# Kernel optimization log

Measured on AMD Instinct MI355X. Metric: run time of the kernel, lower is better.

Reference implementation:

```python
import jax, jax.numpy as jnp
import numpy as np


def setup_inputs() -> dict:
    key = jax.random.key(0)
    k1, k2 = jax.random.split(key)
    b, c, h, w = 8, 256, 96, 192
    x = jax.random.normal(k1, (b, c, h, w), dtype=jnp.float32)
    y = jax.random.normal(k2, (b, c, h, w), dtype=jnp.float32)
    return {"x": x, "y": y, "max_displacement": 4}


def _correlation(x, y, md):
    # x, y: [B, C, H, W]. Output: [B, K*K, H, W], K = 2*md+1.
    b, c, h, w = x.shape
    K = 2 * md + 1
    # zero-pad y spatially so out-of-bounds displacements contribute 0
    yp = jnp.pad(y, ((0, 0), (0, 0), (md, md), (md, md)))
    # fixed small loop over K*K displacements (81 for md=4)
    outs = [
        jnp.einsum('bchw,bchw->bhw', x, yp[:, :, di:di + h, dj:dj + w])
        for di in range(K) for dj in range(K)
    ]
    out = jnp.stack(outs, axis=1)  # [B, K*K, H, W]
    return out / c


def reference(x, y, max_displacement):
    return _correlation(x, y, max_displacement)
```

## Files before the change

kernel.cpp:

```cpp
#include <hip/hip_runtime.h>
#include <hip/hip_bf16.h>
#include <stdint.h>


using f32x4 = __attribute__((ext_vector_type(4))) float;
using s16x4 = __attribute__((ext_vector_type(4))) short;
using u16x4 = __attribute__((ext_vector_type(4))) unsigned short;

#define C_DIM 256
#define H_DIM 96
#define W_DIM 192
#define HWSZ  (H_DIM * W_DIM)
#define MD 4
#define KD 9
#define CHUNK 16
#define NCHUNK (C_DIM / CHUNK)
#define HR 8
#define NTHR 512
#define WTILES 12
#define HQ 12
#define SUB_B 128
#define YROW_B (8 * SUB_B)
#define XROW_B (4 * SUB_B)
#define YSZ    (16 * YROW_B)
#define XBASE  YSZ
#define BUFSZ  (YSZ + 8 * XROW_B)
#define LDS_BYTES (2 * BUFSZ)

static __device__ __forceinline__ unsigned short bf16b(float f) {
  __bf16 h = (__bf16)f;
  unsigned short s; __builtin_memcpy(&s, &h, 2); return s;
}

static __device__ __forceinline__ s16x4 tr16(uint32_t addr) {
  s16x4 d;
  asm volatile("ds_read_b64_tr_b16 %0, %1" : "=v"(d) : "v"(addr));
  return d;
}

__global__ __launch_bounds__(NTHR, 4)
void corr_mfma(const float* __restrict__ xg, const float* __restrict__ yg,
               float* __restrict__ outg) {
  __shared__ __align__(16) char smem[LDS_BYTES];

  const int bid = blockIdx.x;
  const int b   = bid & 7;
  const int rem = bid >> 3;
  const int wt  = rem / HQ;
  const int hq  = rem - wt * HQ;
  const int w0  = wt * 16;
  const int h0  = hq * HR;

  const int tid  = threadIdx.x;
  const int lane = tid & 63;
  const int wv   = tid >> 6;
  const int hi   = lane >> 4;
  const int lm   = lane & 15;

  const uint32_t sbase = (uint32_t)(uintptr_t)&smem[0];

  uint32_t goffY[3], loffY[3], goffX, loffX;
  uint32_t vmY = 0;
#pragma unroll
  for (int i = 0; i < 3; ++i) {
    const int qid = i * NTHR + tid;
    const int q = qid % 6;
    const int c = (qid / 6) & 15;
    const int r = qid / 96;
    const int hg = h0 + r - MD;
    const int sg = w0 - MD + 4 * q;
    const bool ok = (hg >= 0) && (hg < H_DIM) && (sg >= 0) && (sg < W_DIM);
    if (ok) vmY |= (1u << i);
    goffY[i] = ok ? (uint32_t)(((b * C_DIM + c) * H_DIM + hg) * W_DIM + sg) : 0u;
    const int s = 4 * q;
    loffY[i] = r * YROW_B + (s >> 4) * 512 + (c >> 2) * SUB_B + (c & 3) * 32 + (s & 15) * 2;
  }
  {
    const int q = tid & 3;
    const int c = (tid >> 2) & 15;
    const int r = tid >> 6;
    goffX = (uint32_t)(((b * C_DIM + c) * H_DIM + (h0 + r)) * W_DIM + (w0 + 4 * q));
    loffX = XBASE + r * XROW_B + (c >> 2) * SUB_B + (c & 3) * 32 + 8 * q;
  }

  f32x4 acc[KD][2];
#pragma unroll
  for (int di = 0; di < KD; ++di) {
    acc[di][0] = f32x4{0.f, 0.f, 0.f, 0.f};
    acc[di][1] = f32x4{0.f, 0.f, 0.f, 0.f};
  }

  const uint32_t abase = sbase + XBASE + wv * XROW_B + hi * SUB_B + lm * 8;
  const uint32_t bbase = sbase + wv * YROW_B + hi * SUB_B + lm * 8;

  float4 v[4];
  u16x4  wreg[4];

#pragma unroll
  for (int i = 0; i < 3; ++i) {
    float4 t4 = make_float4(0.f, 0.f, 0.f, 0.f);
    if (vmY & (1u << i)) t4 = *(const float4*)(yg + goffY[i]);
    v[i] = t4;
  }
  v[3] = *(const float4*)(xg + goffX);
#pragma unroll
  for (int i = 0; i < 4; ++i)
    wreg[i] = u16x4{bf16b(v[i].x), bf16b(v[i].y), bf16b(v[i].z), bf16b(v[i].w)};
#pragma unroll
  for (int i = 0; i < 3; ++i) *(u16x4*)(smem + loffY[i]) = wreg[i];
  *(u16x4*)(smem + loffX) = wreg[3];
  __syncthreads();

  for (int t = 0; t < NCHUNK; ++t) {
    if (t + 1 < NCHUNK) {
      const uint32_t co = (uint32_t)(t + 1) * CHUNK * HWSZ;
#pragma unroll
      for (int i = 0; i < 3; ++i) {
        float4 t4 = make_float4(0.f, 0.f, 0.f, 0.f);
        if (vmY & (1u << i)) t4 = *(const float4*)(yg + goffY[i] + co);
        v[i] = t4;
      }
      v[3] = *(const float4*)(xg + goffX + co);
    }

    const uint32_t bo = (uint32_t)(t & 1) * BUFSZ;
    s16x4 afr = tr16(abase + bo);
    s16x4 b0 = tr16(bbase + bo);
    s16x4 b1 = tr16(bbase + bo + 512);
#pragma unroll
    for (int di = 0; di < KD; ++di) {
      s16x4 n0, n1;
      if (di < 8) {
        const uint32_t bb = bbase + bo + (uint32_t)(di + 1) * YROW_B;
        n0 = tr16(bb);
        n1 = tr16(bb + 512);
        asm volatile("s_waitcnt lgkmcnt(2)" ::: "memory");
      } else {
        asm volatile("s_waitcnt lgkmcnt(0)" ::: "memory");
      }
      __builtin_amdgcn_sched_barrier(0);
      acc[di][0] = __builtin_amdgcn_mfma_f32_16x16x16bf16_1k(afr, b0, acc[di][0], 0, 0, 0);
      acc[di][1] = __builtin_amdgcn_mfma_f32_16x16x16bf16_1k(afr, b1, acc[di][1], 0, 0, 0);
      if (di < 8) { b0 = n0; b1 = n1; }
    }

    if (t + 1 < NCHUNK) {
#pragma unroll
      for (int i = 0; i < 4; ++i)
        wreg[i] = u16x4{bf16b(v[i].x), bf16b(v[i].y), bf16b(v[i].z), bf16b(v[i].w)};
      __syncthreads();
      const uint32_t wo = (uint32_t)((t + 1) & 1) * BUFSZ;
#pragma unroll
      for (int i = 0; i < 3; ++i) *(u16x4*)(smem + wo + loffY[i]) = wreg[i];
      *(u16x4*)(smem + wo + loffX) = wreg[3];
      __syncthreads();
    }
  }

  const int h = h0 + wv;
  const float scale = 1.f / 256.f;
#pragma unroll
  for (int di = 0; di < KD; ++di) {
#pragma unroll
    for (int t = 0; t < 2; ++t) {
#pragma unroll
      for (int rg = 0; rg < 4; ++rg) {
        const int m = hi * 4 + rg;
        const int dj = t * 16 + lm - m;
        if (0 <= dj && dj <= 8) {
          outg[((b * (KD * KD) + di * KD + dj) * H_DIM + h) * W_DIM + w0 + m] =
              acc[di][t][rg] * scale;
        }
      }
    }
  }
}

extern "C" void kernel_launch(void* const* d_in, const int* in_sizes, int n_in,
                              void* d_out, int out_size, void* d_ws, size_t ws_size,
                              hipStream_t stream) {
  const float* x = (const float*)d_in[0];
  const float* y = (const float*)d_in[1];
  float* out = (float*)d_out;
  (void)in_sizes; (void)n_in; (void)d_ws; (void)ws_size; (void)out_size;

  const int grid = 8 * HQ * WTILES;
  corr_mfma<<<dim3(grid), dim3(NTHR), 0, stream>>>(x, y, out);
}
```

Before: 156.5 us.

## Deepen LDS fragment prefetch, raise wave priority, and drop a barrier per chunk

The inner MFMA loop is unrolled by hand so up to four pairs of transposed B-fragment LDS reads are in flight, with explicit lgkmcnt waits tuned to that depth. The MFMA section is wrapped in s_setprio to favour issuing matrix work. The double-buffered LDS refill now needs only the trailing __syncthreads each chunk instead of two, which removes one block-wide barrier per iteration. This raises VGPR pressure from the extra in-flight fragments, and correctness depends on the hand-counted waitcnt values.

```diff
diff --git a/kernel.cpp b/kernel.cpp
--- a/kernel.cpp
+++ b/kernel.cpp
@@ -14,7 +14,7 @@
 #define MD 4
 #define KD 9
 #define CHUNK 16
-#define NCHUNK (C_DIM / CHUNK)
+#define NCHUNK 16
 #define HR 8
 #define NTHR 512
 #define WTILES 12
@@ -22,9 +22,8 @@
 #define SUB_B 128
 #define YROW_B (8 * SUB_B)
 #define XROW_B (4 * SUB_B)
-#define YSZ    (16 * YROW_B)
-#define XBASE  YSZ
-#define BUFSZ  (YSZ + 8 * XROW_B)
+#define XBASE  (16 * YROW_B)
+#define BUFSZ  (XBASE + 8 * XROW_B)
 #define LDS_BYTES (2 * BUFSZ)
 
 static __device__ __forceinline__ unsigned short bf16b(float f) {
@@ -37,6 +36,8 @@
   asm volatile("ds_read_b64_tr_b16 %0, %1" : "=v"(d) : "v"(addr));
   return d;
 }
+
+#define WAITLG(n) asm volatile("s_waitcnt lgkmcnt(" #n ")" ::: "memory")
 
 __global__ __launch_bounds__(NTHR, 4)
 void corr_mfma(const float* __restrict__ xg, const float* __restrict__ yg,
@@ -93,25 +94,24 @@
   const uint32_t abase = sbase + XBASE + wv * XROW_B + hi * SUB_B + lm * 8;
   const uint32_t bbase = sbase + wv * YROW_B + hi * SUB_B + lm * 8;
 
-  float4 v[4];
-  u16x4  wreg[4];
-
-#pragma unroll
-  for (int i = 0; i < 3; ++i) {
-    float4 t4 = make_float4(0.f, 0.f, 0.f, 0.f);
-    if (vmY & (1u << i)) t4 = *(const float4*)(yg + goffY[i]);
-    v[i] = t4;
-  }
-  v[3] = *(const float4*)(xg + goffX);
-#pragma unroll
-  for (int i = 0; i < 4; ++i)
-    wreg[i] = u16x4{bf16b(v[i].x), bf16b(v[i].y), bf16b(v[i].z), bf16b(v[i].w)};
-#pragma unroll
-  for (int i = 0; i < 3; ++i) *(u16x4*)(smem + loffY[i]) = wreg[i];
-  *(u16x4*)(smem + loffX) = wreg[3];
+  {
+    float4 v[4];
+#pragma unroll
+    for (int i = 0; i < 3; ++i) {
+      float4 t4 = make_float4(0.f, 0.f, 0.f, 0.f);
+      if (vmY & (1u << i)) t4 = *(const float4*)(yg + goffY[i]);
+      v[i] = t4;
+    }
+    v[3] = *(const float4*)(xg + goffX);
+#pragma unroll
+    for (int i = 0; i < 3; ++i)
+      *(u16x4*)(smem + loffY[i]) = u16x4{bf16b(v[i].x), bf16b(v[i].y), bf16b(v[i].z), bf16b(v[i].w)};
+    *(u16x4*)(smem + loffX) = u16x4{bf16b(v[3].x), bf16b(v[3].y), bf16b(v[3].z), bf16b(v[3].w)};
+  }
   __syncthreads();
 
   for (int t = 0; t < NCHUNK; ++t) {
+    float4 v[4];
     if (t + 1 < NCHUNK) {
       const uint32_t co = (uint32_t)(t + 1) * CHUNK * HWSZ;
 #pragma unroll
@@ -124,37 +124,53 @@
     }
 
     const uint32_t bo = (uint32_t)(t & 1) * BUFSZ;
-    s16x4 afr = tr16(abase + bo);
-    s16x4 b0 = tr16(bbase + bo);
-    s16x4 b1 = tr16(bbase + bo + 512);
-#pragma unroll
-    for (int di = 0; di < KD; ++di) {
-      s16x4 n0, n1;
-      if (di < 8) {
-        const uint32_t bb = bbase + bo + (uint32_t)(di + 1) * YROW_B;
-        n0 = tr16(bb);
-        n1 = tr16(bb + 512);
-        asm volatile("s_waitcnt lgkmcnt(2)" ::: "memory");
-      } else {
-        asm volatile("s_waitcnt lgkmcnt(0)" ::: "memory");
-      }
-      __builtin_amdgcn_sched_barrier(0);
-      acc[di][0] = __builtin_amdgcn_mfma_f32_16x16x16bf16_1k(afr, b0, acc[di][0], 0, 0, 0);
-      acc[di][1] = __builtin_amdgcn_mfma_f32_16x16x16bf16_1k(afr, b1, acc[di][1], 0, 0, 0);
-      if (di < 8) { b0 = n0; b1 = n1; }
-    }
+    s16x4 afr;
+    s16x4 bf[4][2];
+
+#define ISSUE_PAIR(slot, row) \
+    bf[(slot) & 3][0] = tr16(bbase + bo + (uint32_t)(row) * YROW_B); \
+    bf[(slot) & 3][1] = tr16(bbase + bo + (uint32_t)(row) * YROW_B + 512);
+
+#define DO_DI(di, lg) \
+    WAITLG(lg); __builtin_amdgcn_sched_barrier(0); \
+    acc[di][0] = __builtin_amdgcn_mfma_f32_16x16x16bf16_1k(afr, bf[(di) & 3][0], acc[di][0], 0, 0, 0); \
+    acc[di][1] = __builtin_amdgcn_mfma_f32_16x16x16bf16_1k(afr, bf[(di) & 3][1], acc[di][1], 0, 0, 0);
+
+    __builtin_amdgcn_s_setprio(1);
+    afr = tr16(abase + bo);
+    ISSUE_PAIR(0, 0)
+    ISSUE_PAIR(1, 1)
+    ISSUE_PAIR(2, 2)
+    ISSUE_PAIR(3, 3)
+    DO_DI(0, 6)
+    ISSUE_PAIR(4, 4)
+    DO_DI(1, 6)
+    ISSUE_PAIR(5, 5)
+    DO_DI(2, 6)
+    ISSUE_PAIR(6, 6)
+    DO_DI(3, 6)
+    ISSUE_PAIR(7, 7)
+    DO_DI(4, 6)
+    ISSUE_PAIR(8, 8)
+    DO_DI(5, 6)
+    DO_DI(6, 4)
+    DO_DI(7, 2)
+    DO_DI(8, 0)
+    __builtin_amdgcn_s_setprio(0);
+
+#undef ISSUE_PAIR
+#undef DO_DI
 
     if (t + 1 < NCHUNK) {
-#pragma unroll
-      for (int i = 0; i < 4; ++i)
-        wreg[i] = u16x4{bf16b(v[i].x), bf16b(v[i].y), bf16b(v[i].z), bf16b(v[i].w)};
-      __syncthreads();
       const uint32_t wo = (uint32_t)((t + 1) & 1) * BUFSZ;
 #pragma unroll
-      for (int i = 0; i < 3; ++i) *(u16x4*)(smem + wo + loffY[i]) = wreg[i];
-      *(u16x4*)(smem + wo + loffX) = wreg[3];
-      __syncthreads();
-    }
+      for (int i = 0; i < 3; ++i)
+        *(u16x4*)(smem + wo + loffY[i]) =
+            u16x4{bf16b(v[i].x), bf16b(v[i].y), bf16b(v[i].z), bf16b(v[i].w)};
+      *(u16x4*)(smem + wo + loffX) =
+          u16x4{bf16b(v[3].x), bf16b(v[3].y), bf16b(v[3].z), bf16b(v[3].w)};
+    }
+    __syncthreads();
   }
 
   const int h = h0 + wv;
```

New measurement: 156.3 us. About the same (-0.1%).

## Shrink tile to two rows, split displacement rows across waves, load x directly

Applied to the files above, without the earlier changes.

Each block now handles two output rows with 256 threads instead of eight rows with 512, quadrupling the grid. Each wave pair covers five of the nine vertical displacements (rows 0-4 and 4-8), so row 4 is computed twice. The A operand (x) is read straight from global memory into registers instead of being staged in LDS. The inner loop now issues all B-fragment LDS reads up front, raises wave priority around the MFMAs, and uses a single barrier per chunk instead of two. This trades more redundant y-halo loading (10 rows per 2 output rows) and uncoalesced scalar x loads for more parallelism, less LDS, and fewer syncs.

```diff
diff --git a/kernel.cpp b/kernel.cpp
--- a/kernel.cpp
+++ b/kernel.cpp
@@ -14,18 +14,16 @@
 #define MD 4
 #define KD 9
 #define CHUNK 16
-#define NCHUNK (C_DIM / CHUNK)
-#define HR 8
-#define NTHR 512
+#define NCHUNK 16
+#define NTHR 256
 #define WTILES 12
-#define HQ 12
+#define HQ 48
 #define SUB_B 128
 #define YROW_B (8 * SUB_B)
-#define XROW_B (4 * SUB_B)
-#define YSZ    (16 * YROW_B)
-#define XBASE  YSZ
-#define BUFSZ  (YSZ + 8 * XROW_B)
+#define NROWS 10
+#define BUFSZ (NROWS * YROW_B)
 #define LDS_BYTES (2 * BUFSZ)
+#define NYQ (NROWS * CHUNK * 6)
 
 static __device__ __forceinline__ unsigned short bf16b(float f) {
   __bf16 h = (__bf16)f;
@@ -37,6 +35,8 @@
   asm volatile("ds_read_b64_tr_b16 %0, %1" : "=v"(d) : "v"(addr));
   return d;
 }
+
+#define WAITLG(n) asm volatile("s_waitcnt lgkmcnt(" #n ")" ::: "memory")
 
 __global__ __launch_bounds__(NTHR, 4)
 void corr_mfma(const float* __restrict__ xg, const float* __restrict__ yg,
@@ -49,127 +49,138 @@
   const int wt  = rem / HQ;
   const int hq  = rem - wt * HQ;
   const int w0  = wt * 16;
-  const int h0  = hq * HR;
+  const int h0  = hq * 2;
 
   const int tid  = threadIdx.x;
   const int lane = tid & 63;
   const int wv   = tid >> 6;
+  const int hh   = wv & 1;
+  const int dh   = wv >> 1;
   const int hi   = lane >> 4;
   const int lm   = lane & 15;
 
   const uint32_t sbase = (uint32_t)(uintptr_t)&smem[0];
 
-  uint32_t goffY[3], loffY[3], goffX, loffX;
+  uint32_t goffY[4], loffY[4];
   uint32_t vmY = 0;
-#pragma unroll
-  for (int i = 0; i < 3; ++i) {
+  uint32_t exY = 0;
+#pragma unroll
+  for (int i = 0; i < 4; ++i) {
     const int qid = i * NTHR + tid;
-    const int q = qid % 6;
-    const int c = (qid / 6) & 15;
-    const int r = qid / 96;
-    const int hg = h0 + r - MD;
-    const int sg = w0 - MD + 4 * q;
-    const bool ok = (hg >= 0) && (hg < H_DIM) && (sg >= 0) && (sg < W_DIM);
-    if (ok) vmY |= (1u << i);
-    goffY[i] = ok ? (uint32_t)(((b * C_DIM + c) * H_DIM + hg) * W_DIM + sg) : 0u;
-    const int s = 4 * q;
-    loffY[i] = r * YROW_B + (s >> 4) * 512 + (c >> 2) * SUB_B + (c & 3) * 32 + (s & 15) * 2;
-  }
+    if (qid < NYQ) {
+      exY |= (1u << i);
+      const int q = qid % 6;
+      const int c = (qid / 6) & 15;
+      const int r = qid / 96;
+      const int hg = h0 + r - MD;
+      const int sg = w0 - MD + 4 * q;
+      const bool ok = (hg >= 0) && (hg < H_DIM) && (sg >= 0) && (sg < W_DIM);
+      if (ok) vmY |= (1u << i);
+      goffY[i] = ok ? (uint32_t)(((b * C_DIM + c) * H_DIM + hg) * W_DIM + sg) : 0u;
+      const int s = 4 * q;
+      loffY[i] = r * YROW_B + (s >> 4) * 512 + (c >> 2) * SUB_B + (c & 3) * 32 + (s & 15) * 2;
+    } else {
+      goffY[i] = 0u; loffY[i] = 0u;
+    }
+  }
+
+  const int h = h0 + hh;
+  uint32_t xoff[4];
+#pragma unroll
+  for (int e = 0; e < 4; ++e)
+    xoff[e] = (uint32_t)(((b * C_DIM + hi * 4 + e) * H_DIM + h) * W_DIM + w0 + lm);
+
+  f32x4 acc[5][2];
+#pragma unroll
+  for (int dl = 0; dl < 5; ++dl) {
+    acc[dl][0] = f32x4{0.f, 0.f, 0.f, 0.f};
+    acc[dl][1] = f32x4{0.f, 0.f, 0.f, 0.f};
+  }
+
+  const uint32_t bbase = sbase + (uint32_t)(hh + dh * 4) * YROW_B + hi * SUB_B + lm * 8;
+
   {
-    const int q = tid & 3;
-    const int c = (tid >> 2) & 15;
-    const int r = tid >> 6;
-    goffX = (uint32_t)(((b * C_DIM + c) * H_DIM + (h0 + r)) * W_DIM + (w0 + 4 * q));
-    loffX = XBASE + r * XROW_B + (c >> 2) * SUB_B + (c & 3) * 32 + 8 * q;
-  }
-
-  f32x4 acc[KD][2];
-#pragma unroll
-  for (int di = 0; di < KD; ++di) {
-    acc[di][0] = f32x4{0.f, 0.f, 0.f, 0.f};
-    acc[di][1] = f32x4{0.f, 0.f, 0.f, 0.f};
-  }
-
-  const uint32_t abase = sbase + XBASE + wv * XROW_B + hi * SUB_B + lm * 8;
-  const uint32_t bbase = sbase + wv * YROW_B + hi * SUB_B + lm * 8;
-
-  float4 v[4];
-  u16x4  wreg[4];
-
-#pragma unroll
-  for (int i = 0; i < 3; ++i) {
-    float4 t4 = make_float4(0.f, 0.f, 0.f, 0.f);
-    if (vmY & (1u << i)) t4 = *(const float4*)(yg + goffY[i]);
-    v[i] = t4;
-  }
-  v[3] = *(const float4*)(xg + goffX);
-#pragma unroll
-  for (int i = 0; i < 4; ++i)
-    wreg[i] = u16x4{bf16b(v[i].x), bf16b(v[i].y), bf16b(v[i].z), bf16b(v[i].w)};
-#pragma unroll
-  for (int i = 0; i < 3; ++i) *(u16x4*)(smem + loffY[i]) = wreg[i];
-  *(u16x4*)(smem + loffX) = wreg[3];
+    float4 v[4];
+#pragma unroll
+    for (int i = 0; i < 4; ++i) {
+      float4 t4 = make_float4(0.f, 0.f, 0.f, 0.f);
+      if (vmY & (1u << i)) t4 = *(const float4*)(yg + goffY[i]);
+      v[i] = t4;
+    }
+#pragma unroll
+    for (int i = 0; i < 4; ++i)
+      if (exY & (1u << i))
+        *(u16x4*)(smem + loffY[i]) =
+            u16x4{bf16b(v[i].x), bf16b(v[i].y), bf16b(v[i].z), bf16b(v[i].w)};
+  }
   __syncthreads();
 
   for (int t = 0; t < NCHUNK; ++t) {
+    const uint32_t co = (uint32_t)t * CHUNK * HWSZ;
+
+    float xa0 = xg[xoff[0] + co], xa1 = xg[xoff[1] + co];
+    float xa2 = xg[xoff[2] + co], xa3 = xg[xoff[3] + co];
+    s16x4 afr;
+    afr[0] = (short)bf16b(xa0); afr[1] = (short)bf16b(xa1);
+    afr[2] = (short)bf16b(xa2); afr[3] = (short)bf16b(xa3);
+
+    float4 v[4];
     if (t + 1 < NCHUNK) {
-      const uint32_t co = (uint32_t)(t + 1) * CHUNK * HWSZ;
-#pragma unroll
-      for (int i = 0; i < 3; ++i) {
+      const uint32_t cn = co + CHUNK * HWSZ;
+#pragma unroll
+      for (int i = 0; i < 4; ++i) {
         float4 t4 = make_float4(0.f, 0.f, 0.f, 0.f);
-        if (vmY & (1u << i)) t4 = *(const float4*)(yg + goffY[i] + co);
+        if (vmY & (1u << i)) t4 = *(const float4*)(yg + goffY[i] + cn);
         v[i] = t4;
       }
-      v[3] = *(const float4*)(xg + goffX + co);
     }
 
     const uint32_t bo = (uint32_t)(t & 1) * BUFSZ;
-    s16x4 afr = tr16(abase + bo);
-    s16x4 b0 = tr16(bbase + bo);
-    s16x4 b1 = tr16(bbase + bo + 512);
-#pragma unroll
-    for (int di = 0; di < KD; ++di) {
-      s16x4 n0, n1;
-      if (di < 8) {
-        const uint32_t bb = bbase + bo + (uint32_t)(di + 1) * YROW_B;
-        n0 = tr16(bb);
-        n1 = tr16(bb + 512);
-        asm volatile("s_waitcnt lgkmcnt(2)" ::: "memory");
-      } else {
-        asm volatile("s_waitcnt lgkmcnt(0)" ::: "memory");
-      }
-      __builtin_amdgcn_sched_barrier(0);
-      acc[di][0] = __builtin_amdgcn_mfma_f32_16x16x16bf16_1k(afr, b0, acc[di][0], 0, 0, 0);
-      acc[di][1] = __builtin_amdgcn_mfma_f32_16x16x16bf16_1k(afr, b1, acc[di][1], 0, 0, 0);
-      if (di < 8) { b0 = n0; b1 = n1; }
-    }
+    s16x4 bf[5][2];
+#pragma unroll
+    for (int dl = 0; dl < 5; ++dl) {
+      bf[dl][0] = tr16(bbase + bo + (uint32_t)dl * YROW_B);
+      bf[dl][1] = tr16(bbase + bo + (uint32_t)dl * YROW_B + 512);
+    }
+
+#define DO_DI(dl, lg) \
+    WAITLG(lg); __builtin_amdgcn_sched_barrier(0); \
+    acc[dl][0] = __builtin_amdgcn_mfma_f32_16x16x16bf16_1k(afr, bf[dl][0], acc[dl][0], 0, 0, 0); \
+    acc[dl][1] = __builtin_amdgcn_mfma_f32_16x16x16bf16_1k(afr, bf[dl][1], acc[dl][1], 0, 0, 0);
+
+    __builtin_amdgcn_s_setprio(1);
+    DO_DI(0, 8)
+    DO_DI(1, 6)
+    DO_DI(2, 4)
+    DO_DI(3, 2)
+    DO_DI(4, 0)
+    __builtin_amdgcn_s_setprio(0);
+#undef DO_DI
 
     if (t + 1 < NCHUNK) {
+      const uint32_t wo = (uint32_t)((t + 1) & 1) * BUFSZ;
 #pragma unroll
       for (int i = 0; i < 4; ++i)
-        wreg[i] = u16x4{bf16b(v[i].x), bf16b(v[i].y), bf16b(v[i].z), bf16b(v[i].w)};
-      __syncthreads();
-      const uint32_t wo = (uint32_t)((t + 1) & 1) * BUFSZ;
-#pragma unroll
-      for (int i = 0; i < 3; ++i) *(u16x4*)(smem + wo + loffY[i]) = wreg[i];
-      *(u16x4*)(smem + wo + loffX) = wreg[3];
-      __syncthreads();
-    }
-  }
-
-  const int h = h0 + wv;
+        if (exY & (1u << i))
+          *(u16x4*)(smem + wo + loffY[i]) =
+              u16x4{bf16b(v[i].x), bf16b(v[i].y), bf16b(v[i].z), bf16b(v[i].w)};
+    }
+    __syncthreads();
+  }
+
   const float scale = 1.f / 256.f;
 #pragma unroll
-  for (int di = 0; di < KD; ++di) {
-#pragma unroll
-    for (int t = 0; t < 2; ++t) {
+  for (int dl = 0; dl < 5; ++dl) {
+    const int di = dh * 4 + dl;
+#pragma unroll
+    for (int tt = 0; tt < 2; ++tt) {
 #pragma unroll
       for (int rg = 0; rg < 4; ++rg) {
         const int m = hi * 4 + rg;
-        const int dj = t * 16 + lm - m;
+        const int dj = tt * 16 + lm - m;
         if (0 <= dj && dj <= 8) {
           outg[((b * (KD * KD) + di * KD + dj) * H_DIM + h) * W_DIM + w0 + m] =
-              acc[di][t][rg] * scale;
+              acc[dl][tt][rg] * scale;
         }
       }
     }
```

New measurement: 184.0 us. 17.6% more time.
